# Performance work log

Measured on AMD Instinct MI355X. Metric: run time of the kernel, lower is better.

Reference implementation:

```python
import jax, jax.numpy as jnp
import numpy as np
from math import factorial

# ---------------- real Wigner-3j coefficients (l <= 2) ----------------

def _w3j_c(l1, l2, l3, m1, m2, m3):
    if m1 + m2 + m3 != 0:
        return 0.0
    f = factorial
    pref = ((-1.0) ** (l1 - l2 - m3)) * np.sqrt(
        f(l1 + l2 - l3) * f(l1 - l2 + l3) * f(-l1 + l2 + l3) / f(l1 + l2 + l3 + 1)
        * f(l1 + m1) * f(l1 - m1) * f(l2 + m2) * f(l2 - m2) * f(l3 + m3) * f(l3 - m3))
    s = 0.0
    for t in range(0, l1 + l2 - l3 + 1):
        ds = [t, l3 - l2 + t + m1, l3 - l1 + t - m2, l1 + l2 - l3 - t, l1 - t - m1, l2 - t + m2]
        if min(ds) < 0:
            continue
        den = 1
        for d in ds:
            den *= f(d)
        s += ((-1.0) ** t) / den
    return pref * s

def _u_real(l):
    # complex->real spherical-harmonic change of basis (rows: mu=-l..l, cols: m=-l..l)
    U = np.zeros((2 * l + 1, 2 * l + 1), dtype=np.complex128)
    U[l, l] = 1.0
    for m in range(1, l + 1):
        U[l + m, l + m] = ((-1) ** m) / np.sqrt(2)
        U[l + m, l - m] = 1.0 / np.sqrt(2)
        U[l - m, l - m] = 1j / np.sqrt(2)
        U[l - m, l + m] = -1j * ((-1) ** m) / np.sqrt(2)
    return U

def _real_w3j(l1, l2, l3):
    W = np.zeros((2 * l1 + 1, 2 * l2 + 1, 2 * l3 + 1), dtype=np.complex128)
    for a, m1 in enumerate(range(-l1, l1 + 1)):
        for b, m2 in enumerate(range(-l2, l2 + 1)):
            for c, m3 in enumerate(range(-l3, l3 + 1)):
                W[a, b, c] = _w3j_c(l1, l2, l3, m1, m2, m3)
    C = np.einsum('am,bn,co,mno->abc', _u_real(l1), _u_real(l2), _u_real(l3), W)
    C = C.real + C.imag  # each entry is purely real or purely imaginary
    n = np.linalg.norm(C)
    if n > 0:
        C = C / n
    return jnp.asarray(C, dtype=jnp.float32)

W3J = {(l1, l2, l3): _real_w3j(l1, l2, l3)
       for l1 in range(3) for l2 in range(3) for l3 in range(3)
       if abs(l1 - l2) <= l3 <= l1 + l2}

SH_OFF = [0, 1, 4]
RELU_GAIN = float(np.sqrt(2.0))  # normalize2mom gain for ReLU

# ---------------- building blocks ----------------

def tp_instructions(in_ls):
    # input irrep blocks have parity (-1)**l (0e,1o,2e); sh = 0e+1o+2e; out = 0e+1o+2e
    ins = []
    for i1, l1 in enumerate(in_ls):
        for l2 in range(3):
            for l3 in range(3):
                if abs(l1 - l2) <= l3 <= l1 + l2 and ((-1) ** (l1 + l2)) == (-1) ** l3:
                    ins.append((i1, l1, l2, l3))
    return ins

def sh_l2(d):
    # component-normalized real spherical harmonics of unit vectors, l=0..2
    x, y, z = d[:, 0], d[:, 1], d[:, 2]
    s3, s15, s5 = np.sqrt(3.0), np.sqrt(15.0), np.sqrt(5.0)
    sh0 = jnp.ones_like(x)[:, None]
    sh1 = jnp.stack([s3 * y, s3 * z, s3 * x], axis=1)
    sh2 = jnp.stack([s15 * x * y, s15 * y * z, (s5 / 2) * (3 * z * z - 1.0),
                     s15 * x * z, (s15 / 2) * (x * x - y * y)], axis=1)
    return jnp.concatenate([sh0, sh1, sh2], axis=1)

def radial_basis(d, num=11, start=0.0, end=8.0):
    values = jnp.linspace(start, end, num)
    step = values[1] - values[0]
    diff = (d[:, None] - values) / step
    return jnp.exp(-(diff * diff)) / 1.12  # e3nn soft_one_hot_linspace 'gaussian'

def radial_net(rb, w1, w2):
    h = jax.nn.relu(rb @ (w1 / np.sqrt(w1.shape[0]))) * RELU_GAIN
    return h @ (w2 / np.sqrt(w2.shape[0]))

def equiv_conv(pos, x, src, dst, rw1, rw2, in_ls, mul_in, C):
    E = src.shape[0]
    vec = pos[src] - pos[dst]                      # (E,3)
    dist = jnp.sqrt(jnp.sum(vec * vec, axis=1))    # (E,)
    w = radial_net(radial_basis(dist), rw1, rw2)   # (E, weight_numel)
    dirs = vec / jnp.maximum(dist, 1e-12)[:, None]
    sh = sh_l2(dirs)                               # (E,9)
    xd = x[dst]                                    # edge gather
    ins = tp_instructions(in_ls)
    fan = {0: 0, 1: 0, 2: 0}
    for (_, l1, l2, l3) in ins:
        fan[l3] += mul_in
    in_off = np.cumsum([0] + [mul_in * (2 * l + 1) for l in in_ls])
    out = [jnp.zeros((E, C, 2 * l3 + 1), x.dtype) for l3 in range(3)]
    woff = 0
    for (i1, l1, l2, l3) in ins:
        x1 = xd[:, in_off[i1]:in_off[i1 + 1]].reshape(E, mul_in, 2 * l1 + 1)
        shb = sh[:, SH_OFF[l2]:SH_OFF[l2] + 2 * l2 + 1]
        wi = w[:, woff:woff + mul_in * C].reshape(E, mul_in, C)
        woff += mul_in * C
        alpha = np.sqrt(2 * l3 + 1) / np.sqrt(fan[l3])
        out[l3] = out[l3] + alpha * jnp.einsum('eui,ej,euw,ijk->ewk', x1, shb, wi, W3J[(l1, l2, l3)])
    msg = jnp.concatenate([o.reshape(E, -1) for o in out], axis=1)
    return jax.ops.segment_sum(msg, src, num_segments=pos.shape[0])  # scatter_add onto src

def self_interaction(x, W, mul_in):
    # x: mul_in x (0e+1o+2e); W: (3, mul_in, mul_out)
    outs, off = [], 0
    for l in range(3):
        d = 2 * l + 1
        b = x[:, off:off + mul_in * d].reshape(-1, mul_in, d)
        off += mul_in * d
        outs.append((jnp.einsum('nui,uw->nwi', b, W[l]) / np.sqrt(mul_in)).reshape(x.shape[0], -1))
    return jnp.concatenate(outs, axis=1)

def pointwise_nonlin(x, b, mul):
    outs, off = [], 0
    for l in range(3):
        d = 2 * l + 1
        blk = x[:, off:off + mul * d]
        off += mul * d
        if l == 0:
            outs.append(jax.nn.softplus(blk + b[0]))
        else:
            v = blk.reshape(-1, mul, d)
            gate = jax.nn.softplus(jnp.sqrt(jnp.sum(v * v, axis=2) + 1e-24) + b[l])
            outs.append((v * gate[:, :, None]).reshape(x.shape[0], -1))
    return jnp.concatenate(outs, axis=1)

def pointwise_norm(x):
    return x / (jnp.linalg.norm(x, axis=1, keepdims=True) + 1e-6)

def backbone(pos, features, edge_index, si0_w, c1_rw1, c1_rw2, si1_w, nl1_b,
             c2_rw1, c2_rw2, si2_w, nl2_b, c3_rw1, c3_rw2, si3_w, nl3_b, fsi_w):
    src, dst = edge_index[0], edge_index[1]
    x = features @ si0_w / np.sqrt(features.shape[1])          # 64x0e -> 128x0e
    x = equiv_conv(pos, x, src, dst, c1_rw1, c1_rw2, [0], 128, 128)
    x = pointwise_norm(x)
    x = self_interaction(x, si1_w, 128)
    x = pointwise_nonlin(x, nl1_b, 128)
    x = equiv_conv(pos, x, src, dst, c2_rw1, c2_rw2, [0, 1, 2], 128, 64)
    x = pointwise_norm(x)
    x = self_interaction(x, si2_w, 64)
    x = pointwise_nonlin(x, nl2_b, 64)
    x = equiv_conv(pos, x, src, dst, c3_rw1, c3_rw2, [0, 1, 2], 64, 32)
    x = pointwise_norm(x)
    x = self_interaction(x, si3_w, 32)
    x = pointwise_nonlin(x, nl3_b, 32)
    x = self_interaction(x, fsi_w, 32)
    return x[:, :32]  # scalar (0e) part

# ---------------- harness ----------------

N_NODES, N_EDGES, FEAT = 512, 2048, 64

def setup_inputs() -> dict:
    key = jax.random.key(0)
    ks = jax.random.split(key, 20)
    src = jax.random.randint(ks[0], (N_EDGES,), 0, N_NODES)
    # avoid self-loops (zero-length edges are degenerate for normalize/grad)
    dst = (src + 1 + jax.random.randint(ks[1], (N_EDGES,), 0, N_NODES - 1)) % N_NODES
    edge_index = jnp.stack([src, dst]).astype(jnp.int64)
    rn = lambda k, s: jax.random.normal(k, s, dtype=jnp.float32)
    return {
        'pos': rn(ks[2], (N_NODES, 3)),
        'features': rn(ks[3], (N_NODES, FEAT)),
        'edge_index': edge_index,
        'si0_w': rn(ks[4], (FEAT, 128)),
        'c1_rw1': rn(ks[5], (11, 12)), 'c1_rw2': rn(ks[6], (12, 3 * 128 * 128)),
        'si1_w': rn(ks[7], (3, 128, 128)), 'nl1_b': jnp.zeros((3,), jnp.float32),
        'c2_rw1': rn(ks[8], (11, 12)), 'c2_rw2': rn(ks[9], (12, 11 * 128 * 64)),
        'si2_w': rn(ks[10], (3, 64, 64)), 'nl2_b': jnp.zeros((3,), jnp.float32),
        'c3_rw1': rn(ks[11], (11, 12)), 'c3_rw2': rn(ks[12], (12, 11 * 64 * 32)),
        'si3_w': rn(ks[13], (3, 32, 32)), 'nl3_b': jnp.zeros((3,), jnp.float32),
        'fsi_w': rn(ks[14], (3, 32, 32)),
    }

def reference(pos, features, edge_index, si0_w, c1_rw1, c1_rw2, si1_w, nl1_b,
              c2_rw1, c2_rw2, si2_w, nl2_b, c3_rw1, c3_rw2, si3_w, nl3_b, fsi_w):
    return backbone(pos, features, edge_index, si0_w, c1_rw1, c1_rw2, si1_w, nl1_b,
                    c2_rw1, c2_rw2, si2_w, nl2_b, c3_rw1, c3_rw2, si3_w, nl3_b, fsi_w)
```

## Files before the change

### kernel.cpp

```cpp
#include <hip/hip_runtime.h>
#include <cmath>
#include <cstdint>

#define NNODES 512
#define NEDGES 2048

typedef _Float16 half2v __attribute__((ext_vector_type(2)));

#define OFF_W3J   0
#define OFF_SH    512
#define OFF_H1    (OFF_SH + NEDGES*9)
#define OFF_H2    (OFF_H1 + NEDGES*6)
#define OFF_H3    (OFF_H2 + NEDGES*6)
#define OFF_W2P1  (OFF_H3 + NEDGES*6)
#define OFF_W2P2  (OFF_W2P1 + 6*49152)
#define OFF_W2P3  (OFF_W2P2 + 6*90112)
#define OFF_XH    (OFF_W2P3 + 6*22528)
#define OFF_XB    (OFF_XH + NNODES*576)
#define OFF_MSGA  (OFF_XB + NNODES*1152)
#define OFF_CNT   (OFF_MSGA + NEDGES*576)
#define OFF_COFF  (OFF_CNT + 512)
#define OFF_LIST  (OFF_COFF + 1024)
#define OFF_RANK  (OFF_LIST + 2048)
#define OFF_MSGB  (OFF_RANK + 2048)
#define WS_NEED_SPLIT ((size_t)(OFF_MSGB + NEDGES*576) * 4)

__device__ __forceinline__ unsigned int packh2f(float a, float b){
  half2v h; h.x=(_Float16)a; h.y=(_Float16)b;
  return __builtin_bit_cast(unsigned int, h);
}
__device__ __forceinline__ half2v u2h2(unsigned int u){ return __builtin_bit_cast(half2v, u); }
__device__ __forceinline__ float dot2f(unsigned int a, unsigned int b, float c){
#if __has_builtin(__builtin_amdgcn_fdot2)
  return __builtin_amdgcn_fdot2(u2h2(a), u2h2(b), c, false);
#else
  half2v ha=u2h2(a), hb=u2h2(b);
  return c + (float)ha.x*(float)hb.x + (float)ha.y*(float)hb.y;
#endif
}
__device__ __forceinline__ unsigned int pk2(float a, float b){
#if __has_builtin(__builtin_amdgcn_cvt_pkrtz)
  auto h=__builtin_amdgcn_cvt_pkrtz(a,b);
  return __builtin_bit_cast(unsigned int,h);
#else
  return packh2f(a,b);
#endif
}
__device__ __forceinline__ unsigned short f2h(float f){
  _Float16 h=(_Float16)f; return __builtin_bit_cast(unsigned short,h);
}
__device__ __forceinline__ float softplusf(float v){ return fmaxf(v,0.f)+log1pf(expf(-fabsf(v))); }

__device__ double dfact(int n){ double f=1.0; for(int i=2;i<=n;++i) f*=(double)i; return f; }

__device__ double w3j_c_dev(int l1,int l2,int l3,int m1,int m2,int m3){
  if (m1+m2+m3 != 0) return 0.0;
  int p = l1 - l2 - m3;
  double sign = (((p%2)+2)%2) ? -1.0 : 1.0;
  double pref = sign*sqrt(dfact(l1+l2-l3)*dfact(l1-l2+l3)*dfact(-l1+l2+l3)/dfact(l1+l2+l3+1)
              *dfact(l1+m1)*dfact(l1-m1)*dfact(l2+m2)*dfact(l2-m2)*dfact(l3+m3)*dfact(l3-m3));
  double s=0.0;
  for (int t=0;t<=l1+l2-l3;++t){
    int d0=t, d1v=l3-l2+t+m1, d2v=l3-l1+t-m2, d3v=l1+l2-l3-t, d4=l1-t-m1, d5=l2-t+m2;
    if (d0<0||d1v<0||d2v<0||d3v<0||d4<0||d5<0) continue;
    double den=dfact(d0)*dfact(d1v)*dfact(d2v)*dfact(d3v)*dfact(d4)*dfact(d5);
    s += ((t&1)?-1.0:1.0)/den;
  }
  return pref*s;
}

__device__ void u_real_dev(int l, double Ur[5][5], double Ui[5][5]){
  for(int a=0;a<5;++a)for(int b=0;b<5;++b){Ur[a][b]=0.0;Ui[a][b]=0.0;}
  Ur[l][l]=1.0;
  double inv2 = 1.0/sqrt(2.0);
  for(int m=1;m<=l;++m){
    double sgn = (m&1)?-1.0:1.0;
    Ur[l+m][l+m] = sgn*inv2;
    Ur[l+m][l-m] = inv2;
    Ui[l-m][l-m] = inv2;
    Ui[l-m][l+m] = -sgn*inv2;
  }
}

__global__ void w3j_kernel(float* __restrict__ out){
  const int L1[11]={0,0,0,1,1,1,1,2,2,2,2};
  const int L2[11]={0,1,2,0,1,1,2,0,1,2,2};
  const int L3[11]={0,1,2,1,0,2,1,2,1,0,2};
  const int OFF[11]={0,1,10,35,44,53,98,143,168,213,238};
  int t = blockIdx.x;
  int tid = threadIdx.x;
  int l1=L1[t], l2=L2[t], l3=L3[t];
  int d1=2*l1+1, d2=2*l2+1, d3=2*l3+1;
  int sz=d1*d2*d3;
  __shared__ double Wt[125];
  __shared__ double U1r[5][5],U1i[5][5],U2r[5][5],U2i[5][5],U3r[5][5],U3i[5][5];
  __shared__ double Cv[125];
  __shared__ double red[128];
  for(int idx=tid; idx<sz; idx+=128){
    int a=idx/(d2*d3), rem=idx%(d2*d3), b=rem/d3, c=rem%d3;
    Wt[idx]=w3j_c_dev(l1,l2,l3,a-l1,b-l2,c-l3);
  }
  if(tid==0) u_real_dev(l1,U1r,U1i);
  if(tid==1) u_real_dev(l2,U2r,U2i);
  if(tid==2) u_real_dev(l3,U3r,U3i);
  __syncthreads();
  for(int idx=tid; idx<sz; idx+=128){
    int a=idx/(d2*d3), rem=idx%(d2*d3), b=rem/d3, c=rem%d3;
    double cr=0.0, ci=0.0;
    for(int m=0;m<d1;++m)for(int n=0;n<d2;++n){
      double t2r = U1r[a][m]*U2r[b][n]-U1i[a][m]*U2i[b][n];
      double t2i = U1r[a][m]*U2i[b][n]+U1i[a][m]*U2r[b][n];
      if (t2r==0.0 && t2i==0.0) continue;
      for(int o=0;o<d3;++o){
        double wv=Wt[(m*d2+n)*d3+o];
        if (wv==0.0) continue;
        double t3r=t2r*U3r[c][o]-t2i*U3i[c][o];
        double t3i=t2r*U3i[c][o]+t2i*U3r[c][o];
        cr += t3r*wv; ci += t3i*wv;
      }
    }
    Cv[idx]=cr+ci;
  }
  __syncthreads();
  double s=0.0;
  for(int idx=tid; idx<sz; idx+=128) s+=Cv[idx]*Cv[idx];
  red[tid]=s; __syncthreads();
  for(int d=64; d>0; d>>=1){ if(tid<d) red[tid]+=red[tid+d]; __syncthreads(); }
  double nrm = sqrt(red[0]);
  double inv = (nrm>0.0)?1.0/nrm:0.0;
  for(int idx=tid; idx<sz; idx+=128) out[OFF[t]+idx]=(float)(Cv[idx]*inv);
}

__global__ void edge_prep_kernel(const float* __restrict__ pos, const int* __restrict__ ei,
    const float* __restrict__ rw1a, const float* __restrict__ rw1b, const float* __restrict__ rw1c,
    float* __restrict__ sh, unsigned int* __restrict__ h1, unsigned int* __restrict__ h2,
    unsigned int* __restrict__ h3){
  int e = blockIdx.x*blockDim.x+threadIdx.x;
  if (e>=NEDGES) return;
  int s = ei[e], d = ei[NEDGES+e];
  float vx=pos[3*s]-pos[3*d], vy=pos[3*s+1]-pos[3*d+1], vz=pos[3*s+2]-pos[3*d+2];
  float dist=sqrtf(vx*vx+vy*vy+vz*vz);
  float dm = fmaxf(dist,1e-12f);
  float x=vx/dm, y=vy/dm, z=vz/dm;
  const float s3=sqrtf(3.f), s15=sqrtf(15.f), s5=sqrtf(5.f);
  float shv[9];
  shv[0]=1.f; shv[1]=s3*y; shv[2]=s3*z; shv[3]=s3*x;
  shv[4]=s15*x*y; shv[5]=s15*y*z; shv[6]=0.5f*s5*(3.f*z*z-1.f); shv[7]=s15*x*z; shv[8]=0.5f*s15*(x*x-y*y);
  #pragma unroll
  for(int i=0;i<9;++i) sh[e*9+i]=shv[i];
  float rb[11];
  #pragma unroll
  for(int i=0;i<11;++i){ float diff=(dist-0.8f*(float)i)*(1.f/0.8f); rb[i]=expf(-diff*diff)*(1.f/1.12f); }
  const float c1 = 1.f/sqrtf(11.f);
  const float c2 = sqrtf(2.f)/sqrtf(12.f);
  const float* rws[3]={rw1a,rw1b,rw1c};
  unsigned int* outs[3]={h1,h2,h3};
  for(int L=0;L<3;++L){
    float hv[12];
    #pragma unroll
    for(int r=0;r<12;++r){
      float t=0.f;
      #pragma unroll
      for(int k=0;k<11;++k) t+=rb[k]*rws[L][k*12+r];
      t*=c1;
      hv[r]=fmaxf(t,0.f)*c2;
    }
    #pragma unroll
    for(int r2=0;r2<6;++r2) outs[L][e*6+r2]=packh2f(hv[2*r2],hv[2*r2+1]);
  }
}

__global__ void w2pack_kernel(const float* __restrict__ w2, unsigned int* __restrict__ out, int nW){
  int idx=blockIdx.x*256+threadIdx.x;
  if(idx>=6*nW) return;
  int r2=idx/nW, c=idx-r2*nW;
  out[idx]=packh2f(w2[(size_t)(2*r2)*nW+c], w2[(size_t)(2*r2+1)*nW+c]);
}

__global__ void w1pack_kernel(const float* __restrict__ w2, unsigned int* __restrict__ out){
  int idx=blockIdx.x*256+threadIdx.x;
  if(idx>=384*768) return;
  int col=idx/768, rem=idx-col*768;
  int r=rem/64, u2=rem-r*64;
  int i=col>>7, w=col&127;
  size_t s0=(size_t)r*49152 + i*16384 + (2*u2)*128 + w;
  out[idx]=packh2f(w2[s0], w2[s0+128]);
}

__global__ __launch_bounds__(384) void vgemm1_kernel(const unsigned int* __restrict__ xh,
    const unsigned int* __restrict__ w1p, unsigned int* __restrict__ V){
  __shared__ __align__(16) unsigned int s_x[4][64];
  int tid=threadIdx.x;
  int n0=blockIdx.x*4;
  for(int ix=tid; ix<256; ix+=384){ int n=ix>>6, u2=ix&63; s_x[n][u2]=xh[(size_t)(n0+n)*64+u2]; }
  __syncthreads();
  int col=tid;
  float acc[4][12];
  #pragma unroll
  for(int n=0;n<4;++n)
    #pragma unroll
    for(int r=0;r<12;++r) acc[n][r]=0.f;
  const uint4* Wp=(const uint4*)(w1p + (size_t)col*768);
  for(int u4=0;u4<16;++u4){
    uint4 xv[4];
    #pragma unroll
    for(int n=0;n<4;++n) xv[n]=((const uint4*)s_x[n])[u4];
    #pragma unroll
    for(int r=0;r<12;++r){
      uint4 wv=Wp[r*16+u4];
      #pragma unroll
      for(int n=0;n<4;++n){
        acc[n][r]=dot2f(xv[n].x,wv.x,acc[n][r]);
        acc[n][r]=dot2f(xv[n].y,wv.y,acc[n][r]);
        acc[n][r]=dot2f(xv[n].z,wv.z,acc[n][r]);
        acc[n][r]=dot2f(xv[n].w,wv.w,acc[n][r]);
      }
    }
  }
  #pragma unroll
  for(int n=0;n<4;++n)
    #pragma unroll
    for(int r2=0;r2<6;++r2)
      V[((size_t)(n0+n)*384+col)*6+r2]=pk2(acc[n][2*r2],acc[n][2*r2+1]);
}

__global__ __launch_bounds__(384) void conv1_edge_kernel(const unsigned int* __restrict__ V,
    const unsigned int* __restrict__ h1, const float* __restrict__ shb,
    const int* __restrict__ dstp, const float* __restrict__ w3j,
    unsigned int* __restrict__ msgA){
  const int W3O[3]={0,1,10};
  unsigned short* m16=(unsigned short*)msgA;
  int tid=threadIdx.x;
  int col=tid;
  int i=col>>7, w=col&127;
  int d3=2*i+1;
  float alpha=sqrtf((float)(2*i+1))*(1.f/sqrtf(128.f));
  int e0=blockIdx.x*2;
  #pragma unroll
  for(int s=0;s<2;++s){
    int e=e0+s;
    int n=dstp[e];
    const unsigned int* vp=V+((size_t)n*384+col)*6;
    float G=0.f;
    #pragma unroll
    for(int r2=0;r2<6;++r2) G=dot2f(h1[(size_t)e*6+r2], vp[r2], G);
    int base=(i==0)?0:((i==1)?128:512);
    for(int k=0;k<d3;++k){
      float B=0.f;
      for(int j=0;j<d3;++j) B += shb[(size_t)e*9+i*i+j]*w3j[W3O[i]+j*d3+k];
      m16[(size_t)e*1152 + base + w*d3 + k]=f2h(G*B*alpha);
    }
  }
}

__global__ __launch_bounds__(256) void csr_rank_kernel(const int* __restrict__ src,
    int* __restrict__ cnt, int* __restrict__ rankA){
  __shared__ int s_src[NEDGES];
  int tid=threadIdx.x;
  int4* s4=(int4*)s_src;
  const int4* g4=(const int4*)src;
  for(int i=tid;i<NEDGES/4;i+=256) s4[i]=g4[i];
  __syncthreads();
  int e=blockIdx.x*256+tid;
  int s=s_src[e];
  int lt=0, tot=0;
  for(int b=0;b<NEDGES/4;b+=8){
    int4 v[8];
    #pragma unroll
    for(int k=0;k<8;++k) v[k]=s4[b+k];
    #pragma unroll
    for(int k=0;k<8;++k){
      int j0=4*(b+k);
      tot += ((v[k].x==s)?1:0)+((v[k].y==s)?1:0)+((v[k].z==s)?1:0)+((v[k].w==s)?1:0);
      lt  += ((v[k].x==s&&j0<e)?1:0)+((v[k].y==s&&j0+1<e)?1:0)+((v[k].z==s&&j0+2<e)?1:0)+((v[k].w==s&&j0+3<e)?1:0);
    }
  }
  rankA[e]=lt;
  if(lt==tot-1) cnt[s]=tot;
}

__global__ void csr_scan_kernel(const int* __restrict__ cnt, int* __restrict__ coff){
  __shared__ int s[NNODES];
  int tid=threadIdx.x;
  s[tid]=cnt[tid];
  __syncthreads();
  for(int d=1;d<NNODES;d<<=1){
    int v=(tid>=d)?s[tid-d]:0;
    __syncthreads();
    s[tid]+=v;
    __syncthreads();
  }
  coff[tid+1]=s[tid];
  if(tid==0) coff[0]=0;
}

__global__ void csr_scatter_kernel(const int* __restrict__ src, const int* __restrict__ coff,
    const int* __restrict__ rankA, int* __restrict__ list){
  int e=blockIdx.x*256+threadIdx.x;
  int s=src[e];
  list[coff[s]+rankA[e]]=e;
}

__global__ void si0_kernel(const float* __restrict__ feat, const float* __restrict__ w,
                           unsigned int* __restrict__ xh){
  __shared__ float s_f[64];
  __shared__ unsigned short s_v[128];
  int n=blockIdx.x, tid=threadIdx.x;
  if(tid<64) s_f[tid]=feat[n*64+tid];
  __syncthreads();
  float acc=0.f;
  for(int u=0;u<64;++u) acc += s_f[u]*w[u*128+tid];
  s_v[tid]=f2h(acc*0.125f);
  __syncthreads();
  if(tid<64) xh[(size_t)n*64+tid]=((unsigned int)s_v[2*tid+1]<<16)|s_v[2*tid];
}

struct CInstr { int l1,l2,l3,woff,w3off; float alpha; };
struct LayerArg { CInstr ins[3][4]; int cnt[3]; int gOf[8]; int rank[8]; int nxg[3]; };

template<int MUL,int C,int EB,int NL,int USPLIT,int D3,int L1v>
__device__ __forceinline__ void instr_body(
  const unsigned int* __restrict__ W2h, int nW, int woff,
  const unsigned int (&hreg)[EB][6],
  const uint4* s_xp4, const float* sB,
  float (&acc)[EB][D3], int ubase, int uOff2, int w)
{
  constexpr int D1=2*L1v+1;
  constexpr int MULZ=MUL/USPLIT;
  constexpr int MZ2=MULZ/2;
  constexpr int UC=256/C;
  constexpr int CHZ=MUL/(UC*USPLIT);
  constexpr int CB=(L1v==0)?0:((L1v==1)?MZ2:4*MZ2);
  static_assert(EB==4,"EB must be 4");
  static_assert(CHZ>=2 && (CHZ&1)==0,"CHZ even");
  const unsigned int* Wp = W2h + (size_t)woff + (size_t)ubase*C + w;
  float a2[EB][D1];
  #pragma unroll
  for(int e=0;e<EB;++e){
    #pragma unroll
    for(int i=0;i<D1;++i) a2[e][i]=0.f;
  }
  #pragma unroll 2
  for(int u2=0;u2<CHZ/2;++u2){
    unsigned int wv0[6],wv1[6];
    #pragma unroll
    for(int r=0;r<6;++r){
      wv0[r]=Wp[(size_t)r*nW + (size_t)(2*u2)*C];
      wv1[r]=Wp[(size_t)r*nW + (size_t)(2*u2+1)*C];
    }
    unsigned int wi2[EB];
    #pragma unroll
    for(int e=0;e<EB;++e){
      float w0=0.f,w1=0.f;
      #pragma unroll
      for(int r=0;r<6;++r){ w0=dot2f(hreg[e][r],wv0[r],w0); w1=dot2f(hreg[e][r],wv1[r],w1); }
      wi2[e]=pk2(w0,w1);
    }
    #pragma unroll
    for(int i=0;i<D1;++i){
      uint4 xv = s_xp4[CB + i*MZ2 + uOff2 + u2];
      a2[0][i]=dot2f(wi2[0],xv.x,a2[0][i]);
      a2[1][i]=dot2f(wi2[1],xv.y,a2[1][i]);
      a2[2][i]=dot2f(wi2[2],xv.z,a2[2][i]);
      a2[3][i]=dot2f(wi2[3],xv.w,a2[3][i]);
    }
  }
  #pragma unroll
  for(int e=0;e<EB;++e){
    #pragma unroll
    for(int k=0;k<D3;++k){
      float s=0.f;
      #pragma unroll
      for(int i=0;i<D1;++i) s += a2[e][i]*sB[e*25+i*5+k];
      acc[e][k]+=s;
    }
  }
}

template<int MUL,int C,int EB,int NL,int USPLIT,int D3,int NINS>
__device__ __forceinline__ void conv_main(
  const unsigned int* __restrict__ W2h, int nW,
  const unsigned int (&hreg)[EB][6],
  const uint4* s_xp4, const float* s_B, float* s_red, unsigned short* s_msg,
  unsigned int* __restrict__ msg, const LayerArg& la, int g, int e0,
  int w, int uc, int ubase, int uOff2)
{
  constexpr int UC=256/C;
  const int tid=threadIdx.x;
  float acc[EB][D3];
  #pragma unroll
  for(int e=0;e<EB;++e){
    #pragma unroll
    for(int k=0;k<D3;++k) acc[e][k]=0.f;
  }
  #pragma unroll
  for(int ii=0;ii<NINS;++ii){
    const int l1v=la.ins[g][ii].l1;
    const int woff=la.ins[g][ii].woff;
    switch(l1v){
      case 0: instr_body<MUL,C,EB,NL,USPLIT,D3,0>(W2h,nW,woff,hreg,s_xp4,s_B+ii*EB*25,acc,ubase,uOff2,w); break;
      case 1: instr_body<MUL,C,EB,NL,USPLIT,D3,1>(W2h,nW,woff,hreg,s_xp4,s_B+ii*EB*25,acc,ubase,uOff2,w); break;
      default: instr_body<MUL,C,EB,NL,USPLIT,D3,2>(W2h,nW,woff,hreg,s_xp4,s_B+ii*EB*25,acc,ubase,uOff2,w); break;
    }
  }
  constexpr int L3v=(D3-1)/2;
  constexpr int base32=(L3v==0)?0:((L3v==1)?C/2:2*C);
  constexpr int seg32=C*D3/2;
  for(int e=0;e<EB;++e){
    #pragma unroll
    for(int k=0;k<D3;++k) s_red[k*256+tid]=acc[e][k];
    __syncthreads();
    if(uc==0){
      #pragma unroll
      for(int k=0;k<D3;++k){
        float s=0.f;
        #pragma unroll
        for(int c2=0;c2<UC;++c2) s+=s_red[k*256+c2*C+w];
        s_msg[(e*C+w)*D3+k]=f2h(s);
      }
    }
    __syncthreads();
  }
  const unsigned int* sm32=(const unsigned int*)s_msg;
  for(int ix=tid; ix<EB*seg32; ix+=256){
    int e=ix/seg32, o=ix-e*seg32;
    msg[(size_t)(e0+e)*(9*C/2) + base32 + o] = sm32[e*seg32+o];
  }
}

template<int MUL,int C,int EB,int NL,int USPLIT>
__global__ __launch_bounds__(256,4) void conv_kernel(
  const unsigned int* __restrict__ xh, const unsigned int* __restrict__ W2h, int nW,
  const unsigned int* __restrict__ hb, const float* __restrict__ shb,
  const int* __restrict__ dstp, const float* __restrict__ w3j,
  unsigned int* __restrict__ msg0, unsigned int* __restrict__ msg1, LayerArg la)
{
  constexpr int MUL2=MUL/2;
  constexpr int MULZ=MUL/USPLIT;
  constexpr int MZ2=MULZ/2;
  constexpr int ROW=(NL==1)?MUL2:9*MUL2;
  constexpr int SROW=(NL==1)?MZ2:9*MZ2;
  constexpr int UC=256/C;
  constexpr int CHZ=MUL/(UC*USPLIT);
  constexpr int NB=NEDGES/EB;
  __shared__ unsigned int s_xp[SROW*EB];
  __shared__ float s_B[4*EB*25];
  __shared__ float s_red[5*256];
  __shared__ unsigned short s_msg[EB*C*5];
  int tid=threadIdx.x;
  int bid=blockIdx.x;
  int xcd=bid&7, slot=bid>>3;
  int g=la.gOf[xcd];
  int idx=slot*la.nxg[g]+la.rank[xcd];
  if(idx>=NB*USPLIT) return;
  int zz=idx/NB, et=idx-zz*NB;
  int e0=et*EB;
  unsigned int* msg=(zz==0)?msg0:msg1;
  for(int ix=tid; ix<EB*SROW; ix+=256){
    int e=ix/SROW, c=ix-(ix/SROW)*SROW;
    int l1,i,u2l;
    if(NL==1){ l1=0;i=0;u2l=c; }
    else{
      if(c<MZ2){l1=0;i=0;u2l=c;}
      else if(c<4*MZ2){int t=c-MZ2;i=t/MZ2;u2l=t-i*MZ2;l1=1;}
      else{int t=c-4*MZ2;i=t/MZ2;u2l=t-i*MZ2;l1=2;}
    }
    int gb=(l1==0)?0:((l1==1)?MUL2:4*MUL2);
    int dn=dstp[e0+e];
    s_xp[c*EB+e]=xh[(size_t)dn*ROW + gb + i*MUL2 + zz*MZ2 + u2l];
  }
  int nIns=la.cnt[g];
  for(int ix=tid; ix<nIns*EB*25; ix+=256){
    int ii=ix/(EB*25); int rem=ix%(EB*25); int e=rem/25; int q=rem%25;
    int i=q/5,k=q%5;
    CInstr I=la.ins[g][ii];
    int d1=2*I.l1+1,d2=2*I.l2+1,d3v=2*I.l3+1;
    float v=0.f;
    if(i<d1&&k<d3v){
      int sho=I.l2*I.l2;
      for(int j=0;j<d2;++j) v+=shb[(size_t)(e0+e)*9+sho+j]*w3j[I.w3off+(i*d2+j)*d3v+k];
      v*=I.alpha;
    }
    s_B[(ii*EB+e)*25+q]=v;
  }
  __syncthreads();
  int w=tid%C, uc=tid/C;
  int ubase=zz*MULZ+uc*CHZ;
  int uOff2=uc*(CHZ/2);
  unsigned int hreg[EB][6];
  #pragma unroll
  for(int e=0;e<EB;++e){
    #pragma unroll
    for(int r=0;r<6;++r) hreg[e][r]=hb[(size_t)(e0+e)*6+r];
  }
  const uint4* s_xp4=(const uint4*)s_xp;
  if(NL==1){
    if(g==0)      conv_main<MUL,C,EB,NL,USPLIT,1,1>(W2h,nW,hreg,s_xp4,s_B,s_red,s_msg,msg,la,g,e0,w,uc,ubase,uOff2);
    else if(g==1) conv_main<MUL,C,EB,NL,USPLIT,3,1>(W2h,nW,hreg,s_xp4,s_B,s_red,s_msg,msg,la,g,e0,w,uc,ubase,uOff2);
    else          conv_main<MUL,C,EB,NL,USPLIT,5,1>(W2h,nW,hreg,s_xp4,s_B,s_red,s_msg,msg,la,g,e0,w,uc,ubase,uOff2);
  }else{
    if(g==0)      conv_main<MUL,C,EB,NL,USPLIT,1,3>(W2h,nW,hreg,s_xp4,s_B,s_red,s_msg,msg,la,g,e0,w,uc,ubase,uOff2);
    else if(g==1) conv_main<MUL,C,EB,NL,USPLIT,3,4>(W2h,nW,hreg,s_xp4,s_B,s_red,s_msg,msg,la,g,e0,w,uc,ubase,uOff2);
    else          conv_main<MUL,C,EB,NL,USPLIT,5,4>(W2h,nW,hreg,s_xp4,s_B,s_red,s_msg,msg,la,g,e0,w,uc,ubase,uOff2);
  }
}

__global__ void aggregate_kernel(const unsigned int* __restrict__ msg0,
                                 const unsigned int* __restrict__ msg1,
                                 const int* __restrict__ coff, const int* __restrict__ list,
                                 float* __restrict__ xout, int W32){
  int n=blockIdx.x;
  int b=coff[n], en=coff[n+1];
  for(int c32=threadIdx.x;c32<W32;c32+=blockDim.x){
    float a0=0.f,a1=0.f;
    for(int j=b;j<en;++j){
      size_t o=(size_t)list[j]*W32+c32;
      half2v p=u2h2(msg0[o]); a0+=(float)p.x; a1+=(float)p.y;
      if(msg1){ half2v q=u2h2(msg1[o]); a0+=(float)q.x; a1+=(float)q.y; }
    }
    xout[(size_t)n*(2*W32)+2*c32]=a0;
    xout[(size_t)n*(2*W32)+2*c32+1]=a1;
  }
}

template<int MUL>
__global__ void post_kernel(const float* __restrict__ xin, const float* __restrict__ siw,
                            const float* __restrict__ nlb, unsigned int* __restrict__ xh){
  constexpr int ROW=9*MUL/2;
  __shared__ float s_in[MUL*9];
  __shared__ unsigned short s_out[MUL*9];
  __shared__ float red[256];
  int n=blockIdx.x, tid=threadIdx.x;
  float ss=0.f;
  for(int c=tid;c<MUL*9;c+=256){ float v=xin[(size_t)n*MUL*9+c]; s_in[c]=v; ss+=v*v; }
  red[tid]=ss; __syncthreads();
  for(int d=128;d>0;d>>=1){ if(tid<d) red[tid]+=red[tid+d]; __syncthreads(); }
  float scale=1.f/(sqrtf(red[0])+1e-6f);
  const float inv=scale/sqrtf((float)MUL);
  float b0=nlb[0], b1=nlb[1], b2=nlb[2];
  for(int p=tid;p<3*MUL;p+=256){
    int l=p/MUL, wo=p%MUL;
    if(l==0){
      const float* Wl=siw;
      float a=0.f;
      for(int u=0;u<MUL;++u) a+=s_in[u]*Wl[(size_t)u*MUL+wo];
      s_out[wo]=f2h(softplusf(a*inv+b0));
    } else if(l==1){
      const float* Wl=siw+(size_t)MUL*MUL;
      float v0=0.f,v1=0.f,v2=0.f;
      for(int u=0;u<MUL;++u){
        float wv=Wl[(size_t)u*MUL+wo];
        int bi=MUL+u*3;
        v0+=s_in[bi]*wv; v1+=s_in[bi+1]*wv; v2+=s_in[bi+2]*wv;
      }
      v0*=inv; v1*=inv; v2*=inv;
      float gate=softplusf(sqrtf(v0*v0+v1*v1+v2*v2+1e-24f)+b1);
      int ob=MUL+wo*3;
      s_out[ob]=f2h(v0*gate); s_out[ob+1]=f2h(v1*gate); s_out[ob+2]=f2h(v2*gate);
    } else {
      const float* Wl=siw+(size_t)2*MUL*MUL;
      float v0=0.f,v1=0.f,v2=0.f,v3=0.f,v4=0.f;
      for(int u=0;u<MUL;++u){
        float wv=Wl[(size_t)u*MUL+wo];
        int bi=4*MUL+u*5;
        v0+=s_in[bi]*wv; v1+=s_in[bi+1]*wv; v2+=s_in[bi+2]*wv; v3+=s_in[bi+3]*wv; v4+=s_in[bi+4]*wv;
      }
      v0*=inv; v1*=inv; v2*=inv; v3*=inv; v4*=inv;
      float gate=softplusf(sqrtf(v0*v0+v1*v1+v2*v2+v3*v3+v4*v4+1e-24f)+b2);
      int ob=4*MUL+wo*5;
      s_out[ob]=f2h(v0*gate); s_out[ob+1]=f2h(v1*gate); s_out[ob+2]=f2h(v2*gate);
      s_out[ob+3]=f2h(v3*gate); s_out[ob+4]=f2h(v4*gate);
    }
  }
  __syncthreads();
  for(int p=tid;p<ROW;p+=256){
    int l,i,u2;
    if(p<MUL/2){l=0;i=0;u2=p;}
    else if(p<2*MUL){int t=p-MUL/2;i=t/(MUL/2);u2=t%(MUL/2);l=1;}
    else{int t=p-2*MUL;i=t/(MUL/2);u2=t%(MUL/2);l=2;}
    int d=2*l+1, sb=MUL*l*l;
    unsigned short a=s_out[sb+(2*u2)*d+i], bb=s_out[sb+(2*u2+1)*d+i];
    xh[(size_t)n*ROW+p]=((unsigned int)bb<<16)|a;
  }
}

__global__ void final_kernel(const unsigned int* __restrict__ xh, const float* __restrict__ fsi,
                             float* __restrict__ out){
  int gid=blockIdx.x*blockDim.x+threadIdx.x;
  if(gid>=NNODES*32) return;
  int n=gid/32, wo=gid%32;
  float s=0.f;
  for(int u2=0;u2<16;++u2){
    half2v p=u2h2(xh[(size_t)n*144+u2]);
    s += (float)p.x*fsi[(2*u2)*32+wo] + (float)p.y*fsi[(2*u2+1)*32+wo];
  }
  out[gid]=s*(1.f/sqrtf(32.f));
}

static int w3off_of(int l1,int l2,int l3){
  const int L1[11]={0,0,0,1,1,1,1,2,2,2,2};
  const int L2[11]={0,1,2,0,1,1,2,0,1,2,2};
  const int L3[11]={0,1,2,1,0,2,1,2,1,0,2};
  const int OFF[11]={0,1,10,35,44,53,98,143,168,213,238};
  for(int i=0;i<11;++i) if(L1[i]==l1&&L2[i]==l2&&L3[i]==l3) return OFF[i];
  return 0;
}

static void fill_map(LayerArg& la, const int alloc[3]){
  int x=0;
  for(int g=0;g<3;++g){
    la.nxg[g]=alloc[g];
    for(int r=0;r<alloc[g];++r){ la.gOf[x]=g; la.rank[x]=r; ++x; }
  }
}
static int gridS(const int alloc[3], int NBZ){
  int S=0;
  for(int g=0;g<3;++g){ int s=(NBZ+alloc[g]-1)/alloc[g]; if(s>S)S=s; }
  return S;
}

extern "C" void kernel_launch(void* const* d_in, const int* in_sizes, int n_in,
                              void* d_out, int out_size, void* d_ws, size_t ws_size,
                              hipStream_t stream) {
  const float* pos    = (const float*)d_in[0];
  const float* feat   = (const float*)d_in[1];
  const int*   ei     = (const int*)d_in[2];
  const float* si0w   = (const float*)d_in[3];
  const float* c1_rw1 = (const float*)d_in[4];
  const float* c1_rw2 = (const float*)d_in[5];
  const float* si1w   = (const float*)d_in[6];
  const float* nl1b   = (const float*)d_in[7];
  const float* c2_rw1 = (const float*)d_in[8];
  const float* c2_rw2 = (const float*)d_in[9];
  const float* si2w   = (const float*)d_in[10];
  const float* nl2b   = (const float*)d_in[11];
  const float* c3_rw1 = (const float*)d_in[12];
  const float* c3_rw2 = (const float*)d_in[13];
  const float* si3w   = (const float*)d_in[14];
  const float* nl3b   = (const float*)d_in[15];
  const float* fsiw   = (const float*)d_in[16];

  float* ws_f=(float*)d_ws;
  float* w3   = ws_f+OFF_W3J;
  float* sh   = ws_f+OFF_SH;
  unsigned int* h1   = (unsigned int*)(ws_f+OFF_H1);
  unsigned int* h2   = (unsigned int*)(ws_f+OFF_H2);
  unsigned int* h3   = (unsigned int*)(ws_f+OFF_H3);
  unsigned int* w2p1 = (unsigned int*)(ws_f+OFF_W2P1);
  unsigned int* w2p2 = (unsigned int*)(ws_f+OFF_W2P2);
  unsigned int* w2p3 = (unsigned int*)(ws_f+OFF_W2P3);
  unsigned int* xh   = (unsigned int*)(ws_f+OFF_XH);
  float* xb   = ws_f+OFF_XB;
  unsigned int* msgA = (unsigned int*)(ws_f+OFF_MSGA);
  unsigned int* msgB = (unsigned int*)(ws_f+OFF_MSGB);
  unsigned int* V    = msgB;
  int* cnt    = (int*)(ws_f+OFF_CNT);
  int* coff   = (int*)(ws_f+OFF_COFF);
  int* clist  = (int*)(ws_f+OFF_LIST);
  int* rankA  = (int*)(ws_f+OFF_RANK);
  const int* src  = ei;
  const int* dstp = ei+NEDGES;

  const bool split = ws_size >= WS_NEED_SPLIT;
  const int NB = NEDGES/4;

  LayerArg la1{}, la2{}, la3{};
  {
    int step=128*128;
    for(int i=0;i<3;++i){
      CInstr I{0,i,i, i*step, w3off_of(0,i,i), (float)std::sqrt((2.0*i+1.0)/128.0)};
      la1.ins[i][la1.cnt[i]++]=I;
    }
  }
  const int insL[11][3]={{0,0,0},{0,1,1},{0,2,2},{1,0,1},{1,1,0},{1,1,2},{1,2,1},{2,0,2},{2,1,1},{2,2,0},{2,2,2}};
  auto build=[&](LayerArg& la, int mul, int Cc){
    int step=mul*Cc;
    int fan[3]={0,0,0};
    for(int i=0;i<11;++i) fan[insL[i][2]] += mul;
    for(int i=0;i<11;++i){
      int l1v=insL[i][0],l2v=insL[i][1],l3v=insL[i][2];
      CInstr I{l1v,l2v,l3v, i*step, w3off_of(l1v,l2v,l3v), (float)std::sqrt((2.0*l3v+1.0)/(double)fan[l3v])};
      la.ins[l3v][la.cnt[l3v]++]=I;
    }
  };
  build(la2,128,64);
  build(la3,64,32);

  const int alloc1[3]={3,3,2};
  const int alloc23[3]={2,3,3};
  fill_map(la1,alloc1);
  fill_map(la2,alloc23);
  fill_map(la3,alloc23);

  w3j_kernel<<<dim3(11),dim3(128),0,stream>>>(w3);
  edge_prep_kernel<<<dim3(NEDGES/256),dim3(256),0,stream>>>(pos,ei,c1_rw1,c2_rw1,c3_rw1, sh,h1,h2,h3);
  if(split){
    w1pack_kernel<<<dim3((384*768+255)/256),dim3(256),0,stream>>>(c1_rw2,w2p1);
  } else {
    w2pack_kernel<<<dim3((6*49152+255)/256),dim3(256),0,stream>>>(c1_rw2,w2p1,49152);
  }
  w2pack_kernel<<<dim3((6*90112+255)/256),dim3(256),0,stream>>>(c2_rw2,w2p2,90112);
  w2pack_kernel<<<dim3((6*22528+255)/256),dim3(256),0,stream>>>(c3_rw2,w2p3,22528);

  hipMemsetAsync(cnt,0,NNODES*sizeof(int),stream);
  csr_rank_kernel<<<dim3(NEDGES/256),dim3(256),0,stream>>>(src,cnt,rankA);
  csr_scan_kernel<<<dim3(1),dim3(NNODES),0,stream>>>(cnt,coff);
  csr_scatter_kernel<<<dim3(NEDGES/256),dim3(256),0,stream>>>(src,coff,rankA,clist);

  si0_kernel<<<dim3(NNODES),dim3(128),0,stream>>>(feat,si0w,xh);

  if(split){
    vgemm1_kernel<<<dim3(NNODES/4),dim3(384),0,stream>>>(xh,w2p1,V);
    conv1_edge_kernel<<<dim3(NEDGES/2),dim3(384),0,stream>>>(V,h1,sh,dstp,w3,msgA);
    aggregate_kernel<<<dim3(NNODES),dim3(256),0,stream>>>(msgA,(const unsigned int*)nullptr,coff,clist,xb,576);
    post_kernel<128><<<dim3(NNODES),dim3(256),0,stream>>>(xb,si1w,nl1b,xh);
    int S23=gridS(alloc23,NB*2);
    conv_kernel<128,64,4,3,2><<<dim3(8*S23),dim3(256),0,stream>>>(xh,w2p2,11*128*64,h2,sh,dstp,w3,msgA,msgB,la2);
    aggregate_kernel<<<dim3(NNODES),dim3(256),0,stream>>>(msgA,msgB,coff,clist,xb,288);
    post_kernel<64><<<dim3(NNODES),dim3(256),0,stream>>>(xb,si2w,nl2b,xh);
    int S3=gridS(alloc23,NB);
    conv_kernel<64,32,4,3,1><<<dim3(8*S3),dim3(256),0,stream>>>(xh,w2p3,11*64*32,h3,sh,dstp,w3,msgA,msgA,la3);
    aggregate_kernel<<<dim3(NNODES),dim3(256),0,stream>>>(msgA,(const unsigned int*)nullptr,coff,clist,xb,144);
    post_kernel<32><<<dim3(NNODES),dim3(256),0,stream>>>(xb,si3w,nl3b,xh);
  } else {
    int S1=gridS(alloc1,NB), S23=gridS(alloc23,NB);
    conv_kernel<128,128,4,1,1><<<dim3(8*S1),dim3(256),0,stream>>>(xh,w2p1,3*128*128,h1,sh,dstp,w3,msgA,msgA,la1);
    aggregate_kernel<<<dim3(NNODES),dim3(256),0,stream>>>(msgA,(const unsigned int*)nullptr,coff,clist,xb,576);
    post_kernel<128><<<dim3(NNODES),dim3(256),0,stream>>>(xb,si1w,nl1b,xh);
    conv_kernel<128,64,4,3,1><<<dim3(8*S23),dim3(256),0,stream>>>(xh,w2p2,11*128*64,h2,sh,dstp,w3,msgA,msgA,la2);
    aggregate_kernel<<<dim3(NNODES),dim3(256),0,stream>>>(msgA,(const unsigned int*)nullptr,coff,clist,xb,288);
    post_kernel<64><<<dim3(NNODES),dim3(256),0,stream>>>(xb,si2w,nl2b,xh);
    conv_kernel<64,32,4,3,1><<<dim3(8*S23),dim3(256),0,stream>>>(xh,w2p3,11*64*32,h3,sh,dstp,w3,msgA,msgA,la3);
    aggregate_kernel<<<dim3(NNODES),dim3(256),0,stream>>>(msgA,(const unsigned int*)nullptr,coff,clist,xb,144);
    post_kernel<32><<<dim3(NNODES),dim3(256),0,stream>>>(xb,si3w,nl3b,xh);
  }

  final_kernel<<<dim3((NNODES*32+255)/256),dim3(256),0,stream>>>(xh,fsiw,(float*)d_out);
}
```

Measured before the change: 335.7 us.

## Interleave radial weights for vector loads, prefetch them, fuse aggregate with post

The packed radial-weight table is split into a 4-wide and a 2-wide interleaved array per column, so the conv inner loop can fetch all six half2 rows with one uint4 and one uint2 load. The next iteration's weights are software-prefetched into registers and the loop is fully unrolled. Separately, the aggregate and post kernels are merged so neighbour sums go straight into shared memory, removing the float scratch buffer round trip and one launch per layer. The costs are higher register pressure from full unrolling and prefetching, and the fused kernel's per-node gather loop now sits in the post kernel.

```diff
diff --git a/kernel.cpp b/kernel.cpp
--- a/kernel.cpp
+++ b/kernel.cpp
@@ -170,11 +170,14 @@
   }
 }
 
-__global__ void w2pack_kernel(const float* __restrict__ w2, unsigned int* __restrict__ out, int nW){
+__global__ void w2packAB_kernel(const float* __restrict__ w2, unsigned int* __restrict__ outA,
+                                unsigned int* __restrict__ outB, int nW){
   int idx=blockIdx.x*256+threadIdx.x;
   if(idx>=6*nW) return;
   int r2=idx/nW, c=idx-r2*nW;
-  out[idx]=packh2f(w2[(size_t)(2*r2)*nW+c], w2[(size_t)(2*r2+1)*nW+c]);
+  unsigned int v=packh2f(w2[(size_t)(2*r2)*nW+c], w2[(size_t)(2*r2+1)*nW+c]);
+  if(r2<4) outA[(size_t)c*4+r2]=v;
+  else     outB[(size_t)c*2+(r2-4)]=v;
 }
 
 __global__ void w1pack_kernel(const float* __restrict__ w2, unsigned int* __restrict__ out){
@@ -320,7 +323,7 @@
 
 template<int MUL,int C,int EB,int NL,int USPLIT,int D3,int L1v>
 __device__ __forceinline__ void instr_body(
-  const unsigned int* __restrict__ W2h, int nW, int woff,
+  const unsigned int* __restrict__ W2A, const unsigned int* __restrict__ W2B, int woff,
   const unsigned int (&hreg)[EB][6],
   const uint4* s_xp4, const float* sB,
   float (&acc)[EB][D3], int ubase, int uOff2, int w)
@@ -333,27 +336,33 @@
   constexpr int CB=(L1v==0)?0:((L1v==1)?MZ2:4*MZ2);
   static_assert(EB==4,"EB must be 4");
   static_assert(CHZ>=2 && (CHZ&1)==0,"CHZ even");
-  const unsigned int* Wp = W2h + (size_t)woff + (size_t)ubase*C + w;
+  const int colb = woff + ubase*C + w;
+  const uint4* WA = ((const uint4*)W2A) + colb;
+  const uint2* WB = ((const uint2*)W2B) + colb;
   float a2[EB][D1];
   #pragma unroll
   for(int e=0;e<EB;++e){
     #pragma unroll
     for(int i=0;i<D1;++i) a2[e][i]=0.f;
   }
-  #pragma unroll 2
+  uint4 pa0=WA[0], pa1=WA[C];
+  uint2 pb0=WB[0], pb1=WB[C];
+  #pragma unroll
   for(int u2=0;u2<CHZ/2;++u2){
-    unsigned int wv0[6],wv1[6];
-    #pragma unroll
-    for(int r=0;r<6;++r){
-      wv0[r]=Wp[(size_t)r*nW + (size_t)(2*u2)*C];
-      wv1[r]=Wp[(size_t)r*nW + (size_t)(2*u2+1)*C];
+    uint4 ca0=pa0, ca1=pa1;
+    uint2 cb0=pb0, cb1=pb1;
+    if(u2+1<CHZ/2){
+      int o=(2*u2+2)*C;
+      pa0=WA[o]; pa1=WA[o+C]; pb0=WB[o]; pb1=WB[o+C];
     }
     unsigned int wi2[EB];
     #pragma unroll
     for(int e=0;e<EB;++e){
       float w0=0.f,w1=0.f;
-      #pragma unroll
-      for(int r=0;r<6;++r){ w0=dot2f(hreg[e][r],wv0[r],w0); w1=dot2f(hreg[e][r],wv1[r],w1); }
+      w0=dot2f(hreg[e][0],ca0.x,w0); w0=dot2f(hreg[e][1],ca0.y,w0); w0=dot2f(hreg[e][2],ca0.z,w0);
+      w0=dot2f(hreg[e][3],ca0.w,w0); w0=dot2f(hreg[e][4],cb0.x,w0); w0=dot2f(hreg[e][5],cb0.y,w0);
+      w1=dot2f(hreg[e][0],ca1.x,w1); w1=dot2f(hreg[e][1],ca1.y,w1); w1=dot2f(hreg[e][2],ca1.z,w1);
+      w1=dot2f(hreg[e][3],ca1.w,w1); w1=dot2f(hreg[e][4],cb1.x,w1); w1=dot2f(hreg[e][5],cb1.y,w1);
       wi2[e]=pk2(w0,w1);
     }
     #pragma unroll
@@ -379,7 +388,7 @@
 
 template<int MUL,int C,int EB,int NL,int USPLIT,int D3,int NINS>
 __device__ __forceinline__ void conv_main(
-  const unsigned int* __restrict__ W2h, int nW,
+  const unsigned int* __restrict__ W2A, const unsigned int* __restrict__ W2B,
   const unsigned int (&hreg)[EB][6],
   const uint4* s_xp4, const float* s_B, float* s_red, unsigned short* s_msg,
   unsigned int* __restrict__ msg, const LayerArg& la, int g, int e0,
@@ -398,9 +407,9 @@
     const int l1v=la.ins[g][ii].l1;
     const int woff=la.ins[g][ii].woff;
     switch(l1v){
-      case 0: instr_body<MUL,C,EB,NL,USPLIT,D3,0>(W2h,nW,woff,hreg,s_xp4,s_B+ii*EB*25,acc,ubase,uOff2,w); break;
-      case 1: instr_body<MUL,C,EB,NL,USPLIT,D3,1>(W2h,nW,woff,hreg,s_xp4,s_B+ii*EB*25,acc,ubase,uOff2,w); break;
-      default: instr_body<MUL,C,EB,NL,USPLIT,D3,2>(W2h,nW,woff,hreg,s_xp4,s_B+ii*EB*25,acc,ubase,uOff2,w); break;
+      case 0: instr_body<MUL,C,EB,NL,USPLIT,D3,0>(W2A,W2B,woff,hreg,s_xp4,s_B+ii*EB*25,acc,ubase,uOff2,w); break;
+      case 1: instr_body<MUL,C,EB,NL,USPLIT,D3,1>(W2A,W2B,woff,hreg,s_xp4,s_B+ii*EB*25,acc,ubase,uOff2,w); break;
+      default: instr_body<MUL,C,EB,NL,USPLIT,D3,2>(W2A,W2B,woff,hreg,s_xp4,s_B+ii*EB*25,acc,ubase,uOff2,w); break;
     }
   }
   constexpr int L3v=(D3-1)/2;
@@ -430,7 +439,8 @@
 
 template<int MUL,int C,int EB,int NL,int USPLIT>
 __global__ __launch_bounds__(256,4) void conv_kernel(
-  const unsigned int* __restrict__ xh, const unsigned int* __restrict__ W2h, int nW,
+  const unsigned int* __restrict__ xh, const unsigned int* __restrict__ W2A,
+  const unsigned int* __restrict__ W2B,
   const unsigned int* __restrict__ hb, const float* __restrict__ shb,
   const int* __restrict__ dstp, const float* __restrict__ w3j,
   unsigned int* __restrict__ msg0, unsigned int* __restrict__ msg1, LayerArg la)
@@ -495,44 +505,40 @@
   }
   const uint4* s_xp4=(const uint4*)s_xp;
   if(NL==1){
-    if(g==0)      conv_main<MUL,C,EB,NL,USPLIT,1,1>(W2h,nW,hreg,s_xp4,s_B,s_red,s_msg,msg,la,g,e0,w,uc,ubase,uOff2);
-    else if(g==1) conv_main<MUL,C,EB,NL,USPLIT,3,1>(W2h,nW,hreg,s_xp4,s_B,s_red,s_msg,msg,la,g,e0,w,uc,ubase,uOff2);
-    else          conv_main<MUL,C,EB,NL,USPLIT,5,1>(W2h,nW,hreg,s_xp4,s_B,s_red,s_msg,msg,la,g,e0,w,uc,ubase,uOff2);
+    if(g==0)      conv_main<MUL,C,EB,NL,USPLIT,1,1>(W2A,W2B,hreg,s_xp4,s_B,s_red,s_msg,msg,la,g,e0,w,uc,ubase,uOff2);
+    else if(g==1) conv_main<MUL,C,EB,NL,USPLIT,3,1>(W2A,W2B,hreg,s_xp4,s_B,s_red,s_msg,msg,la,g,e0,w,uc,ubase,uOff2);
+    else          conv_main<MUL,C,EB,NL,USPLIT,5,1>(W2A,W2B,hreg,s_xp4,s_B,s_red,s_msg,msg,la,g,e0,w,uc,ubase,uOff2);
   }else{
-    if(g==0)      conv_main<MUL,C,EB,NL,USPLIT,1,3>(W2h,nW,hreg,s_xp4,s_B,s_red,s_msg,msg,la,g,e0,w,uc,ubase,uOff2);
-    else if(g==1) conv_main<MUL,C,EB,NL,USPLIT,3,4>(W2h,nW,hreg,s_xp4,s_B,s_red,s_msg,msg,la,g,e0,w,uc,ubase,uOff2);
-    else          conv_main<MUL,C,EB,NL,USPLIT,5,4>(W2h,nW,hreg,s_xp4,s_B,s_red,s_msg,msg,la,g,e0,w,uc,ubase,uOff2);
-  }
-}
-
-__global__ void aggregate_kernel(const unsigned int* __restrict__ msg0,
-                                 const unsigned int* __restrict__ msg1,
-                                 const int* __restrict__ coff, const int* __restrict__ list,
-                                 float* __restrict__ xout, int W32){
-  int n=blockIdx.x;
+    if(g==0)      conv_main<MUL,C,EB,NL,USPLIT,1,3>(W2A,W2B,hreg,s_xp4,s_B,s_red,s_msg,msg,la,g,e0,w,uc,ubase,uOff2);
+    else if(g==1) conv_main<MUL,C,EB,NL,USPLIT,3,4>(W2A,W2B,hreg,s_xp4,s_B,s_red,s_msg,msg,la,g,e0,w,uc,ubase,uOff2);
+    else          conv_main<MUL,C,EB,NL,USPLIT,5,4>(W2A,W2B,hreg,s_xp4,s_B,s_red,s_msg,msg,la,g,e0,w,uc,ubase,uOff2);
+  }
+}
+
+template<int MUL>
+__global__ void agg_post_kernel(const unsigned int* __restrict__ msg0,
+                                const unsigned int* __restrict__ msg1,
+                                const int* __restrict__ coff, const int* __restrict__ list,
+                                const float* __restrict__ siw, const float* __restrict__ nlb,
+                                unsigned int* __restrict__ xh){
+  constexpr int W32=MUL*9/2;
+  constexpr int ROW=9*MUL/2;
+  __shared__ float s_in[MUL*9];
+  __shared__ unsigned short s_out[MUL*9];
+  __shared__ float red[256];
+  int n=blockIdx.x, tid=threadIdx.x;
   int b=coff[n], en=coff[n+1];
-  for(int c32=threadIdx.x;c32<W32;c32+=blockDim.x){
+  float ss=0.f;
+  for(int c32=tid;c32<W32;c32+=256){
     float a0=0.f,a1=0.f;
     for(int j=b;j<en;++j){
       size_t o=(size_t)list[j]*W32+c32;
       half2v p=u2h2(msg0[o]); a0+=(float)p.x; a1+=(float)p.y;
       if(msg1){ half2v q=u2h2(msg1[o]); a0+=(float)q.x; a1+=(float)q.y; }
     }
-    xout[(size_t)n*(2*W32)+2*c32]=a0;
-    xout[(size_t)n*(2*W32)+2*c32+1]=a1;
-  }
-}
-
-template<int MUL>
-__global__ void post_kernel(const float* __restrict__ xin, const float* __restrict__ siw,
-                            const float* __restrict__ nlb, unsigned int* __restrict__ xh){
-  constexpr int ROW=9*MUL/2;
-  __shared__ float s_in[MUL*9];
-  __shared__ unsigned short s_out[MUL*9];
-  __shared__ float red[256];
-  int n=blockIdx.x, tid=threadIdx.x;
-  float ss=0.f;
-  for(int c=tid;c<MUL*9;c+=256){ float v=xin[(size_t)n*MUL*9+c]; s_in[c]=v; ss+=v*v; }
+    s_in[2*c32]=a0; s_in[2*c32+1]=a1;
+    ss+=a0*a0+a1*a1;
+  }
   red[tid]=ss; __syncthreads();
   for(int d=128;d>0;d>>=1){ if(tid<d) red[tid]+=red[tid+d]; __syncthreads(); }
   float scale=1.f/(sqrtf(red[0])+1e-6f);
@@ -649,8 +655,10 @@
   unsigned int* w2p1 = (unsigned int*)(ws_f+OFF_W2P1);
   unsigned int* w2p2 = (unsigned int*)(ws_f+OFF_W2P2);
   unsigned int* w2p3 = (unsigned int*)(ws_f+OFF_W2P3);
+  unsigned int* w2p1A=w2p1,              *w2p1B=w2p1+4*49152;
+  unsigned int* w2p2A=w2p2,              *w2p2B=w2p2+4*90112;
+  unsigned int* w2p3A=w2p3,              *w2p3B=w2p3+4*22528;
   unsigned int* xh   = (unsigned int*)(ws_f+OFF_XH);
-  float* xb   = ws_f+OFF_XB;
   unsigned int* msgA = (unsigned int*)(ws_f+OFF_MSGA);
   unsigned int* msgB = (unsigned int*)(ws_f+OFF_MSGB);
   unsigned int* V    = msgB;
@@ -697,10 +705,10 @@
   if(split){
     w1pack_kernel<<<dim3((384*768+255)/256),dim3(256),0,stream>>>(c1_rw2,w2p1);
   } else {
-    w2pack_kernel<<<dim3((6*49152+255)/256),dim3(256),0,stream>>>(c1_rw2,w2p1,49152);
-  }
-  w2pack_kernel<<<dim3((6*90112+255)/256),dim3(256),0,stream>>>(c2_rw2,w2p2,90112);
-  w2pack_kernel<<<dim3((6*22528+255)/256),dim3(256),0,stream>>>(c3_rw2,w2p3,22528);
+    w2packAB_kernel<<<dim3((6*49152+255)/256),dim3(256),0,stream>>>(c1_rw2,w2p1A,w2p1B,49152);
+  }
+  w2packAB_kernel<<<dim3((6*90112+255)/256),dim3(256),0,stream>>>(c2_rw2,w2p2A,w2p2B,90112);
+  w2packAB_kernel<<<dim3((6*22528+255)/256),dim3(256),0,stream>>>(c3_rw2,w2p3A,w2p3B,22528);
 
   hipMemsetAsync(cnt,0,NNODES*sizeof(int),stream);
   csr_rank_kernel<<<dim3(NEDGES/256),dim3(256),0,stream>>>(src,cnt,rankA);
@@ -712,27 +720,21 @@
   if(split){
     vgemm1_kernel<<<dim3(NNODES/4),dim3(384),0,stream>>>(xh,w2p1,V);
     conv1_edge_kernel<<<dim3(NEDGES/2),dim3(384),0,stream>>>(V,h1,sh,dstp,w3,msgA);
-    aggregate_kernel<<<dim3(NNODES),dim3(256),0,stream>>>(msgA,(const unsigned int*)nullptr,coff,clist,xb,576);
-    post_kernel<128><<<dim3(NNODES),dim3(256),0,stream>>>(xb,si1w,nl1b,xh);
+    agg_post_kernel<128><<<dim3(NNODES),dim3(256),0,stream>>>(msgA,(const unsigned int*)nullptr,coff,clist,si1w,nl1b,xh);
     int S23=gridS(alloc23,NB*2);
-    conv_kernel<128,64,4,3,2><<<dim3(8*S23),dim3(256),0,stream>>>(xh,w2p2,11*128*64,h2,sh,dstp,w3,msgA,msgB,la2);
-    aggregate_kernel<<<dim3(NNODES),dim3(256),0,stream>>>(msgA,msgB,coff,clist,xb,288);
-    post_kernel<64><<<dim3(NNODES),dim3(256),0,stream>>>(xb,si2w,nl2b,xh);
+    conv_kernel<128,64,4,3,2><<<dim3(8*S23),dim3(256),0,stream>>>(xh,w2p2A,w2p2B,h2,sh,dstp,w3,msgA,msgB,la2);
+    agg_post_kernel<64><<<dim3(NNODES),dim3(256),0,stream>>>(msgA,msgB,coff,clist,si2w,nl2b,xh);
     int S3=gridS(alloc23,NB);
-    conv_kernel<64,32,4,3,1><<<dim3(8*S3),dim3(256),0,stream>>>(xh,w2p3,11*64*32,h3,sh,dstp,w3,msgA,msgA,la3);
-    aggregate_kernel<<<dim3(NNODES),dim3(256),0,stream>>>(msgA,(const unsigned int*)nullptr,coff,clist,xb,144);
-    post_kernel<32><<<dim3(NNODES),dim3(256),0,stream>>>(xb,si3w,nl3b,xh);
+    conv_kernel<64,32,4,3,1><<<dim3(8*S3),dim3(256),0,stream>>>(xh,w2p3A,w2p3B,h3,sh,dstp,w3,msgA,msgA,la3);
+    agg_post_kernel<32><<<dim3(NNODES),dim3(256),0,stream>>>(msgA,(const unsigned int*)nullptr,coff,clist,si3w,nl3b,xh);
   } else {
     int S1=gridS(alloc1,NB), S23=gridS(alloc23,NB);
-    conv_kernel<128,128,4,1,1><<<dim3(8*S1),dim3(256),0,stream>>>(xh,w2p1,3*128*128,h1,sh,dstp,w3,msgA,msgA,la1);
-    aggregate_kernel<<<dim3(NNODES),dim3(256),0,stream>>>(msgA,(const unsigned int*)nullptr,coff,clist,xb,576);
-    post_kernel<128><<<dim3(NNODES),dim3(256),0,stream>>>(xb,si1w,nl1b,xh);
-    conv_kernel<128,64,4,3,1><<<dim3(8*S23),dim3(256),0,stream>>>(xh,w2p2,11*128*64,h2,sh,dstp,w3,msgA,msgA,la2);
-    aggregate_kernel<<<dim3(NNODES),dim3(256),0,stream>>>(msgA,(const unsigned int*)nullptr,coff,clist,xb,288);
-    post_kernel<64><<<dim3(NNODES),dim3(256),0,stream>>>(xb,si2w,nl2b,xh);
-    conv_kernel<64,32,4,3,1><<<dim3(8*S23),dim3(256),0,stream>>>(xh,w2p3,11*64*32,h3,sh,dstp,w3,msgA,msgA,la3);
-    aggregate_kernel<<<dim3(NNODES),dim3(256),0,stream>>>(msgA,(const unsigned int*)nullptr,coff,clist,xb,144);
-    post_kernel<32><<<dim3(NNODES),dim3(256),0,stream>>>(xb,si3w,nl3b,xh);
+    conv_kernel<128,128,4,1,1><<<dim3(8*S1),dim3(256),0,stream>>>(xh,w2p1A,w2p1B,h1,sh,dstp,w3,msgA,msgA,la1);
+    agg_post_kernel<128><<<dim3(NNODES),dim3(256),0,stream>>>(msgA,(const unsigned int*)nullptr,coff,clist,si1w,nl1b,xh);
+    conv_kernel<128,64,4,3,1><<<dim3(8*S23),dim3(256),0,stream>>>(xh,w2p2A,w2p2B,h2,sh,dstp,w3,msgA,msgA,la2);
+    agg_post_kernel<64><<<dim3(NNODES),dim3(256),0,stream>>>(msgA,(const unsigned int*)nullptr,coff,clist,si2w,nl2b,xh);
+    conv_kernel<64,32,4,3,1><<<dim3(8*S23),dim3(256),0,stream>>>(xh,w2p3A,w2p3B,h3,sh,dstp,w3,msgA,msgA,la3);
+    agg_post_kernel<32><<<dim3(NNODES),dim3(256),0,stream>>>(msgA,(const unsigned int*)nullptr,coff,clist,si3w,nl3b,xh);
   }
 
   final_kernel<<<dim3((NNODES*32+255)/256),dim3(256),0,stream>>>(xh,fsiw,(float*)d_out);
```

New measurement: 358.3 us. +6.7%, slower.
